# Kernel optimization log

Measured on AMD Instinct MI355X. Metric: run time of the kernel, lower is better.

The kernel has to match this reference:

```python
import jax, jax.numpy as jnp
import numpy as np

N, D, V = 4096, 256, 32000
B, T = 32, 256
U_DECAY, X_DECAY = 0.97, 0.97
EPS = 1e-6


def layernorm_row(z):
    # matches torch: (z - mean) / (std + eps), std with Bessel correction (ddof=1)
    m = jnp.mean(z, axis=-1, keepdims=True)
    s = jnp.std(z, axis=-1, keepdims=True, ddof=1)
    return (z - m) / (s + EPS)


def setup_inputs() -> dict:
    key = jax.random.key(0)
    k1, k2, k3, k4, k5 = jax.random.split(key, 5)
    token_emb = jax.random.normal(k1, (V, D), jnp.float32) / np.float32(np.sqrt(D))
    E = jax.random.normal(k2, (D, N), jnp.float32) / np.float32(np.sqrt(N))
    Dx = jax.random.normal(k3, (N, D), jnp.float32) / np.float32(np.sqrt(D))
    Dy = jax.random.normal(k4, (N, D), jnp.float32) / np.float32(np.sqrt(D))
    idx = jax.random.randint(k5, (B, T), 0, V)
    return {"idx": idx, "token_emb": token_emb, "E": E, "Dx": Dx, "Dy": Dy}


def reference(idx, token_emb, E, Dx, Dy):
    b = idx.shape[0]

    def step(carry, tok):
        x, rho = carry                                   # x: (b,n), rho: (b,d,n)
        v_prev = token_emb[tok]                          # (b,d) embedding gather
        x_t = X_DECAY * x + jax.nn.relu(v_prev @ Dx.T)   # (b,n)
        x_t = x_t / (jnp.sum(jnp.abs(x_t), axis=-1, keepdims=True) + EPS)  # L1 normalize
        a_star = jnp.einsum('bdn,bn->bd', rho, x_t)      # fast-weight readout
        y_t = jax.nn.relu(layernorm_row(a_star) @ Dy.T) * jax.nn.relu(x_t)  # (b,n)
        v_star = layernorm_row(y_t @ E.T)                # (b,d)
        # Hebbian decayed outer-product memory update
        rho = U_DECAY * (rho + jnp.einsum('bd,bn->bdn', layernorm_row(v_prev), x_t))
        return (x_t, rho), v_star

    x0 = jnp.zeros((b, N), jnp.float32)
    rho0 = jnp.zeros((b, D, N), jnp.float32)
    (_, _), vs = jax.lax.scan(step, (x0, rho0), idx.T)   # vs: (T,b,d)
    return jnp.transpose(vs, (1, 0, 2))                  # (b,T,d)
```

## Files before the change

### kernel.cpp

```cpp
#include <hip/hip_runtime.h>
#include <hip/hip_bf16.h>

#define NN 4096
#define DD 256
#define BB 32
#define TT 256
#define EPS 1e-6f
#define DECAY 0.97f
#define LOG2_DECAY -0.043943348f

typedef __hip_bfloat16 bf16;
typedef short short8 __attribute__((ext_vector_type(8)));
typedef float floatx4 __attribute__((ext_vector_type(4)));

__device__ __forceinline__ float bfu2f(short u) {
    return __uint_as_float(((unsigned)(unsigned short)u) << 16);
}

__device__ __forceinline__ float blk_sum_256(float v, volatile float* s4) {
#pragma unroll
    for (int o = 32; o > 0; o >>= 1) v += __shfl_down(v, o, 64);
    int lane = threadIdx.x & 63, w = threadIdx.x >> 6;
    __syncthreads();
    if (lane == 0) s4[w] = v;
    __syncthreads();
    return s4[0] + s4[1] + s4[2] + s4[3];
}

__device__ __forceinline__ void gl16(const bf16* g, bf16* l) {
    __builtin_amdgcn_global_load_lds((const __attribute__((address_space(1))) void*)g,
                                     (__attribute__((address_space(3))) void*)l, 16, 0, 0);
}

__global__ void k_detect(const unsigned short* __restrict__ raw, int* __restrict__ flag) {
    __shared__ int cnt[4];
    int tid = threadIdx.x;
    int bad = 0;
    for (int i = tid; i < 8192; i += 256) {
        unsigned int u = raw[2 * i];
        float v = __uint_as_float(u << 16);
        if (!(fabsf(v) < 1e6f)) bad++;
    }
#pragma unroll
    for (int o = 32; o > 0; o >>= 1) bad += __shfl_down(bad, o, 64);
    int lane = tid & 63, w = tid >> 6;
    if (lane == 0) cnt[w] = bad;
    __syncthreads();
    if (tid == 0) flag[0] = (cnt[0] + cnt[1] + cnt[2] + cnt[3] < 32) ? 1 : 0;
}

__global__ __launch_bounds__(256) void k_convert3(const void* __restrict__ s0,
                                                  const void* __restrict__ s1,
                                                  const void* __restrict__ s2,
                                                  bf16* __restrict__ d0,
                                                  bf16* __restrict__ d1,
                                                  bf16* __restrict__ d2,
                                                  const int* __restrict__ flag) {
    const int per = NN * DD / 8;
    int i = blockIdx.x * 256 + threadIdx.x;
    int m = i / per, j = i % per;
    const void* s = (m == 0) ? s0 : (m == 1) ? s1 : s2;
    bf16* d = (m == 0) ? d0 : (m == 1) ? d1 : d2;
    if (flag[0]) {
        ((uint4*)d)[j] = ((const uint4*)s)[j];
    } else {
        const float4* f = (const float4*)s;
        float4 a = f[2 * j], b = f[2 * j + 1];
        short8 o;
        float va[8] = {a.x, a.y, a.z, a.w, b.x, b.y, b.z, b.w};
#pragma unroll
        for (int k = 0; k < 8; k++) {
            bf16 t = __float2bfloat16(va[k]);
            o[k] = *reinterpret_cast<short*>(&t);
        }
        ((short8*)d)[j] = o;
    }
}

__global__ __launch_bounds__(256) void k_gather_ln(const void* __restrict__ emb,
                                                   const int* __restrict__ idx,
                                                   bf16* __restrict__ Vpb,
                                                   bf16* __restrict__ Ub,
                                                   const int* __restrict__ flag) {
    __shared__ float s4[4];
    int r = blockIdx.x, d = threadIdx.x;
    int tok = idx[r];
    long o = (long)tok * DD + d;
    float e = flag[0] ? __bfloat162float(((const bf16*)emb)[o]) : ((const float*)emb)[o];
    Vpb[(long)r * DD + d] = __float2bfloat16(e);
    float m = blk_sum_256(e, s4) * (1.0f / DD);
    float zc = e - m;
    float var = blk_sum_256(zc * zc, s4) * (1.0f / (DD - 1));
    Ub[(long)r * DD + d] = __float2bfloat16(zc / (sqrtf(fmaxf(var, 0.f)) + EPS));
}

__global__ __launch_bounds__(256) void k_transpose(const bf16* __restrict__ Ub,
                                                   bf16* __restrict__ Ut) {
    __shared__ bf16 tile[32][33];
    int b = blockIdx.z;
    int t0 = blockIdx.x * 32, d0 = blockIdx.y * 32;
    const bf16* src = Ub + (long)b * TT * DD;
    bf16* dst = Ut + (long)b * DD * TT;
    int rr = threadIdx.x >> 3, c4 = (threadIdx.x & 7) * 4;
#pragma unroll
    for (int i = 0; i < 4; i++) tile[rr][c4 + i] = src[(long)(t0 + rr) * DD + d0 + c4 + i];
    __syncthreads();
#pragma unroll
    for (int i = 0; i < 4; i++) dst[(long)(d0 + rr) * TT + t0 + c4 + i] = tile[c4 + i][rr];
}

enum { EPI_RELU_BF16 = 0, EPI_NONE_F32 = 1, EPI_RELU_MULX_BF16 = 2 };

template <int EPI>
__global__ __launch_bounds__(512, 2) void k_fused256(const bf16* __restrict__ A,
                                                     const bf16* __restrict__ B,
                                                     bf16* __restrict__ C,
                                                     const bf16* __restrict__ Xaux,
                                                     float* __restrict__ Wsum) {
    __shared__ __align__(16) char smem[65536];
    bf16* R = (bf16*)smem;

    int bx = blockIdx.x, by = blockIdx.y;
    {
        int gx = gridDim.x;
        int nwg = gx * gridDim.y;
        int id = by * gx + bx;
        int q = nwg >> 3;
        int nid = (id & 7) * q + (id >> 3);
        bx = nid % gx;
        by = nid / gx;
    }
    int bm = by * 256, bn = bx * 256;
    int tid = threadIdx.x, wid = tid >> 6, lane = tid & 63;
    int wr = wid >> 2, wc = wid & 3;
    int lm = lane & 15, kh = lane >> 4;

    int srow2 = tid >> 2;
    int swzcol = (((tid & 3) ^ ((srow2 >> 1) & 3)) << 3);
    const bf16* gA0 = A + (long)(bm + srow2) * DD + swzcol;
    const bf16* gA1 = gA0 + (long)128 * DD;
    const bf16* gB0 = B + (long)(bn + srow2) * DD + swzcol;
    const bf16* gB1 = gB0 + (long)128 * DD;
    int chunk = ((kh ^ ((lm >> 1) & 3)) << 3);

    floatx4 acc[8][4];
#pragma unroll
    for (int i = 0; i < 8; i++)
#pragma unroll
        for (int j = 0; j < 4; j++) acc[i][j] = (floatx4){0.f, 0.f, 0.f, 0.f};

#define STAGE256(SBASE, KK)                             \
    {                                                   \
        bf16* As_ = (bf16*)(SBASE);                     \
        bf16* Bs_ = As_ + 8192;                         \
        gl16(gA0 + (KK), As_ + tid * 8);                \
        gl16(gA1 + (KK), As_ + 4096 + tid * 8);         \
        gl16(gB0 + (KK), Bs_ + tid * 8);                \
        gl16(gB1 + (KK), Bs_ + 4096 + tid * 8);         \
    }

    STAGE256(smem, 0);

    int cur = 0;
#pragma unroll
    for (int k0 = 0; k0 < 256; k0 += 32) {
        __builtin_amdgcn_s_barrier();
        __builtin_amdgcn_sched_barrier(0);
        if (k0 + 32 < 256) STAGE256(smem + ((cur ^ 1) * 32768), k0 + 32);
        if (k0 + 32 < 256) asm volatile("s_waitcnt vmcnt(4)" ::: "memory");
        else               asm volatile("s_waitcnt vmcnt(0)" ::: "memory");
        __builtin_amdgcn_s_barrier();
        __builtin_amdgcn_sched_barrier(0);
        bf16* cbA = (bf16*)(smem + cur * 32768);
        bf16* cbB = cbA + 8192;
        short8 af[8], bfr[4];
#pragma unroll
        for (int i = 0; i < 8; i++)
            af[i] = *(const short8*)(cbA + (wr * 128 + i * 16 + lm) * 32 + chunk);
#pragma unroll
        for (int j = 0; j < 4; j++)
            bfr[j] = *(const short8*)(cbB + (wc * 64 + j * 16 + lm) * 32 + chunk);
#pragma unroll
        for (int i = 0; i < 8; i++)
#pragma unroll
            for (int j = 0; j < 4; j++)
                acc[i][j] = __builtin_amdgcn_mfma_f32_16x16x32_bf16(af[i], bfr[j], acc[i][j], 0, 0, 0);
        cur ^= 1;
    }
#undef STAGE256

#pragma unroll
    for (int p = 0; p < 4; p++) {
        __syncthreads();
        if (wr == (p >> 1)) {
            int ibase = (p & 1) * 4;
#pragma unroll
            for (int ii = 0; ii < 4; ii++)
#pragma unroll
                for (int j = 0; j < 4; j++)
#pragma unroll
                    for (int r = 0; r < 4; r++) {
                        int rr = ii * 16 + kh * 4 + r;
                        int cc = wc * 64 + j * 16 + lm;
                        R[rr * 264 + cc] = __float2bfloat16(fmaxf(acc[ibase + ii][j][r], 0.f));
                    }
        }
        __syncthreads();
#pragma unroll
        for (int it = 0; it < 4; it++) {
            int row_l = it * 16 + (tid >> 5);
            int c8 = (tid & 31) * 8;
            short8 vv = *(const short8*)(R + row_l * 264 + c8);
            int gm = bm + p * 64 + row_l;
            long off = (long)gm * NN + bn + c8;
            if (EPI == EPI_RELU_BF16) {
                *(short8*)(C + off) = vv;
                float s = 0.f;
#pragma unroll
                for (int k = 0; k < 8; k++) s += bfu2f(vv[k]);
#pragma unroll
                for (int o = 16; o > 0; o >>= 1) s += __shfl_down(s, o, 32);
                if ((tid & 31) == 0) atomicAdd(&Wsum[gm], s);
            } else {
                short8 xx = *(const short8*)(Xaux + off);
                short8 oo;
#pragma unroll
                for (int k = 0; k < 8; k++) {
                    float prod = bfu2f(vv[k]) * fmaxf(bfu2f(xx[k]), 0.f);
                    bf16 t = __float2bfloat16(prod);
                    oo[k] = *reinterpret_cast<short*>(&t);
                }
                *(short8*)(C + off) = oo;
            }
        }
    }
}

template <int EPI, int KSPLIT, int TRI, int SWZ>
__global__ __launch_bounds__(256) void k_mfma_nt(int K,
                                                 const bf16* __restrict__ A, int lda, long sA,
                                                 const bf16* __restrict__ B, int ldb, long sB,
                                                 void* __restrict__ Cv, int ldc, long sC,
                                                 const bf16* __restrict__ Xaux,
                                                 float* __restrict__ Wsum) {
    __shared__ __align__(16) char smem[49152];
    bf16* R = (bf16*)smem;

    int z = blockIdx.z;
    int bz = z / KSPLIT, ks = z % KSPLIT;
    A += (long)bz * sA;
    B += (long)bz * sB;
    int bx = blockIdx.x, by = blockIdx.y;
    if (TRI) {
        by = (blockIdx.x >= 1) ? 1 : 0;
        bx = (blockIdx.x == 2) ? 1 : 0;
    }
    if (SWZ) {
        int gx = gridDim.x;
        int nwg = gx * gridDim.y;
        int id = by * gx + bx;
        int q = nwg >> 3;
        int nid = (id & 7) * q + (id >> 3);
        bx = nid % gx;
        by = nid / gx;
    }
    int bm = by * 128, bn = bx * 128;
    int tid = threadIdx.x;
    int srow = tid >> 2;
    int scol = ((((srow >> 1) & 3) ^ (tid & 3)) << 3);
    int w = tid >> 6, lane = tid & 63;
    int wm = (w >> 1) * 64, wn = (w & 1) * 64;
    int lm = lane & 15, kh = lane >> 4;

    floatx4 acc[4][4];
#pragma unroll
    for (int i = 0; i < 4; i++)
#pragma unroll
        for (int j = 0; j < 4; j++) acc[i][j] = (floatx4){0.f, 0.f, 0.f, 0.f};

    int kchunk = K / KSPLIT;
    int kbeg = ks * kchunk, kend = kbeg + kchunk;
    const bf16* gA0 = A + (long)(bm + srow) * lda + scol;
    const bf16* gA1 = gA0 + (long)64 * lda;
    const bf16* gB0 = B + (long)(bn + srow) * ldb + scol;
    const bf16* gB1 = gB0 + (long)64 * ldb;
    int dslot = tid * 8;

#define STAGE_SLOT(SBASE, KK)                          \
    {                                                  \
        bf16* bufA = (bf16*)(SBASE);                   \
        bf16* bufB = bufA + 4096;                      \
        gl16(gA0 + (KK), bufA + dslot);                \
        gl16(gA1 + (KK), bufA + 2048 + dslot);         \
        gl16(gB0 + (KK), bufB + dslot);                \
        gl16(gB1 + (KK), bufB + 2048 + dslot);         \
    }

    STAGE_SLOT(smem, kbeg);
    if (kbeg + 32 < kend) STAGE_SLOT(smem + 16384, kbeg + 32);

    int cur = 0;
    for (int k0 = kbeg; k0 < kend; k0 += 32) {
        __builtin_amdgcn_s_barrier();
        __builtin_amdgcn_sched_barrier(0);
        if (k0 + 64 < kend) {
            int ps = (cur == 0) ? 2 : cur - 1;
            STAGE_SLOT(smem + ps * 16384, k0 + 64);
        }
        int rem = (kend - k0 - 32) >> 5;
        if (rem >= 2)      asm volatile("s_waitcnt vmcnt(8)" ::: "memory");
        else if (rem == 1) asm volatile("s_waitcnt vmcnt(4)" ::: "memory");
        else               asm volatile("s_waitcnt vmcnt(0)" ::: "memory");
        __builtin_amdgcn_s_barrier();
        __builtin_amdgcn_sched_barrier(0);
        bf16* cbA = (bf16*)(smem + cur * 16384);
        bf16* cbB = cbA + 4096;
        short8 af[4], bfr[4];
#pragma unroll
        for (int i = 0; i < 4; i++) {
            int row = wm + i * 16 + lm;
            af[i] = *(const short8*)(cbA + row * 32 + ((((row >> 1) & 3) ^ kh) << 3));
        }
#pragma unroll
        for (int j = 0; j < 4; j++) {
            int row = wn + j * 16 + lm;
            bfr[j] = *(const short8*)(cbB + row * 32 + ((((row >> 1) & 3) ^ kh) << 3));
        }
#pragma unroll
        for (int i = 0; i < 4; i++)
#pragma unroll
            for (int j = 0; j < 4; j++)
                acc[i][j] = __builtin_amdgcn_mfma_f32_16x16x32_bf16(af[i], bfr[j], acc[i][j], 0, 0, 0);
        cur = (cur == 2) ? 0 : cur + 1;
    }
#undef STAGE_SLOT

    if (EPI == EPI_NONE_F32) {
        long cbase = (long)z * sC;
#pragma unroll
        for (int i = 0; i < 4; i++)
#pragma unroll
            for (int j = 0; j < 4; j++)
#pragma unroll
                for (int r = 0; r < 4; r++) {
                    int gm = bm + wm + i * 16 + kh * 4 + r;
                    int gn = bn + wn + j * 16 + lm;
                    ((float*)Cv)[cbase + (long)gm * ldc + gn] = acc[i][j][r];
                }
        return;
    }

#pragma unroll
    for (int p = 0; p < 2; p++) {
        __syncthreads();
        if ((w >> 1) == p) {
#pragma unroll
            for (int i = 0; i < 4; i++)
#pragma unroll
                for (int j = 0; j < 4; j++)
#pragma unroll
                    for (int r = 0; r < 4; r++) {
                        int rr = i * 16 + kh * 4 + r;
                        int cc = wn + j * 16 + lm;
                        R[rr * 136 + cc] = __float2bfloat16(fmaxf(acc[i][j][r], 0.f));
                    }
        }
        __syncthreads();
#pragma unroll
        for (int it = 0; it < 4; it++) {
            int row_l = it * 16 + (tid >> 4);
            int c8 = (tid & 15) * 8;
            short8 vv = *(const short8*)(R + row_l * 136 + c8);
            int gm = bm + p * 64 + row_l;
            long off = (long)gm * ldc + bn + c8;
            if (EPI == EPI_RELU_BF16) {
                *(short8*)((bf16*)Cv + off) = vv;
                float s = 0.f;
#pragma unroll
                for (int k = 0; k < 8; k++) s += bfu2f(vv[k]);
#pragma unroll
                for (int o = 8; o > 0; o >>= 1) s += __shfl_down(s, o, 16);
                if ((tid & 15) == 0) atomicAdd(&Wsum[gm], s);
            } else {
                short8 xx = *(const short8*)(Xaux + off);
                short8 oo;
#pragma unroll
                for (int k = 0; k < 8; k++) {
                    float prod = bfu2f(vv[k]) * fmaxf(bfu2f(xx[k]), 0.f);
                    bf16 t = __float2bfloat16(prod);
                    oo[k] = *reinterpret_cast<short*>(&t);
                }
                *(short8*)((bf16*)Cv + off) = oo;
            }
        }
    }
}

__global__ __launch_bounds__(256) void k_scalar_scan(const float* __restrict__ Wsum,
                                                     float* __restrict__ invS) {
    __shared__ float sw[BB * TT];
    for (int i = threadIdx.x; i < BB * TT; i += 256) sw[i] = Wsum[i];
    __syncthreads();
    int b = threadIdx.x;
    if (b < BB) {
        float sig = 0.f;
        for (int t = 0; t < TT; t++) {
            float S = DECAY * sig + sw[b * TT + t];
            float inv = 1.f / (S + EPS);
            invS[b * TT + t] = inv;
            sig = S * inv;
        }
    }
}

__global__ __launch_bounds__(256) void k_colscan(bf16* __restrict__ W,
                                                 const float* __restrict__ invS) {
    __shared__ float sv[TT];
    int b = blockIdx.y;
    sv[threadIdx.x] = invS[b * TT + threadIdx.x];
    __syncthreads();
    int n = blockIdx.x * 256 + threadIdx.x;
    bf16* p = W + (long)b * TT * NN + n;
    float x = 0.f;
    for (int t = 0; t < TT; t++) {
        float w = __bfloat162float(p[(long)t * NN]);
        x = (DECAY * x + w) * sv[t];
        p[(long)t * NN] = __float2bfloat16(x);
    }
}

__global__ __launch_bounds__(256) void k_reduce_mask(const float* __restrict__ Gp,
                                                     bf16* __restrict__ G) {
    int r = blockIdx.x;
    int b = r >> 8, t = r & 255;
    int s = threadIdx.x;
    long base = ((long)b * 4) * 65536 + (long)t * 256 + s;
    float v = Gp[base] + Gp[base + 65536] + Gp[base + 2 * 65536] + Gp[base + 3 * 65536];
    float o = (s < t) ? v * exp2f((float)(t - s) * LOG2_DECAY) : 0.f;
    G[(long)r * 256 + s] = __float2bfloat16(o);
}

__global__ __launch_bounds__(256) void k_ln_rows(const float* __restrict__ Zp,
                                                 bf16* __restrict__ O) {
    __shared__ float s4[4];
    long r = blockIdx.x;
    int d = threadIdx.x;
    long b = r >> 8, t = r & 255;
    long base = (b * 2) * 65536 + t * 256 + d;
    float z = Zp[base] + Zp[base + 65536];
    float m = blk_sum_256(z, s4) * (1.0f / DD);
    float zc = z - m;
    float var = blk_sum_256(zc * zc, s4) * (1.0f / (DD - 1));
    O[r * DD + d] = __float2bfloat16(zc / (sqrtf(fmaxf(var, 0.f)) + EPS));
}

__global__ __launch_bounds__(256) void k_final_ln(const float* __restrict__ Zp,
                                                  void* __restrict__ out,
                                                  const int* __restrict__ flag) {
    __shared__ float s4[4];
    long r = blockIdx.x;
    int d = threadIdx.x;
    const long SL = (long)8192 * 256;
    long o = r * DD + d;
    float z = Zp[o] + Zp[o + SL] + Zp[o + 2 * SL] + Zp[o + 3 * SL];
    float m = blk_sum_256(z, s4) * (1.0f / DD);
    float zc = z - m;
    float var = blk_sum_256(zc * zc, s4) * (1.0f / (DD - 1));
    float v = zc / (sqrtf(fmaxf(var, 0.f)) + EPS);
    if (flag[0]) ((bf16*)out)[o] = __float2bfloat16(v);
    else ((float*)out)[o] = v;
}

extern "C" void kernel_launch(void* const* d_in, const int* in_sizes, int n_in,
                              void* d_out, int out_size, void* d_ws, size_t ws_size,
                              hipStream_t stream) {
    const int* idx = (const int*)d_in[0];
    const void* emb = d_in[1];
    const void* E = d_in[2];
    const void* Dx = d_in[3];
    const void* Dy = d_in[4];

    char* base = (char*)d_ws;
    size_t off = 0;
    int* flag = (int*)base; off += 1024;
    bf16* Dxb = (bf16*)(base + off); off += (size_t)NN * DD * 2;
    bf16* Dyb = (bf16*)(base + off); off += (size_t)NN * DD * 2;
    bf16* Eb  = (bf16*)(base + off); off += (size_t)DD * NN * 2;
    bf16* Vpb = (bf16*)(base + off); off += (size_t)BB * TT * DD * 2;
    bf16* Ub  = (bf16*)(base + off); off += (size_t)BB * TT * DD * 2;
    bf16* Ut  = (bf16*)(base + off); off += (size_t)BB * TT * DD * 2;
    float* Wsum = (float*)(base + off); off += (size_t)BB * TT * 4;
    float* invS = (float*)(base + off); off += (size_t)BB * TT * 4;
    bf16* ALNb = (bf16*)(base + off); off += (size_t)BB * TT * DD * 2;
    bf16* G = (bf16*)(base + off); off += (size_t)BB * TT * TT * 2;
    float* Gp = (float*)(base + off); off += (size_t)4 * BB * TT * TT * 4;
    float* Astar = Gp;
    float* Zp = Gp;
    bf16* Xb = (bf16*)(base + off); off += (size_t)BB * TT * NN * 2;

    const int M = BB * TT;

    k_detect<<<1, 256, 0, stream>>>((const unsigned short*)emb, flag);
    k_convert3<<<3 * NN * DD / 8 / 256, 256, 0, stream>>>(Dx, Dy, E, Dxb, Dyb, Eb, flag);
    k_gather_ln<<<M, 256, 0, stream>>>(emb, idx, Vpb, Ub, flag);
    k_transpose<<<dim3(8, 8, BB), 256, 0, stream>>>(Ub, Ut);

    hipMemsetAsync(Wsum, 0, (size_t)M * 4, stream);

    k_fused256<EPI_RELU_BF16><<<dim3(16, 32), 512, 0, stream>>>(Vpb, Dxb, Xb, nullptr, Wsum);

    k_scalar_scan<<<1, 256, 0, stream>>>(Wsum, invS);
    k_colscan<<<dim3(16, BB, 1), 256, 0, stream>>>(Xb, invS);

    k_mfma_nt<EPI_NONE_F32, 4, 1, 0><<<dim3(3, 1, BB * 4), 256, 0, stream>>>(
        NN, Xb, NN, (long)TT * NN, Xb, NN, (long)TT * NN, Gp, TT, (long)TT * TT, nullptr, nullptr);
    k_reduce_mask<<<M, 256, 0, stream>>>(Gp, G);

    k_mfma_nt<EPI_NONE_F32, 2, 0, 0><<<dim3(2, 2, BB * 2), 256, 0, stream>>>(
        TT, G, TT, (long)TT * TT, Ut, TT, (long)DD * TT, Astar, DD, (long)TT * DD, nullptr, nullptr);
    k_ln_rows<<<M, 256, 0, stream>>>(Astar, ALNb);

    k_fused256<EPI_RELU_MULX_BF16><<<dim3(16, 32), 512, 0, stream>>>(ALNb, Dyb, Xb, Xb, nullptr);

    k_mfma_nt<EPI_NONE_F32, 4, 0, 1><<<dim3(2, 64, 4), 256, 0, stream>>>(
        NN, Xb, NN, 0, Eb, NN, 0, Zp, DD, (long)M * DD, nullptr, nullptr);

    k_final_ln<<<M, 256, 0, stream>>>(Zp, d_out, flag);
}
```

Before: 312.0 us.

## Deepen fused GEMM pipeline to 4-stage ping-pong and vectorize column scan

The 256x256 fused GEMM goes from double to quad buffering in 128KB of dynamic LDS. Each k-step is split into two MFMA halves, with A and B tile prefetches interleaved between them and s_setprio raising priority around the MFMA blocks, so global loads, LDS reads and matrix math overlap more. The column scan now handles two bf16 columns per thread with 32-bit loads and prefetches the next row. The larger LDS footprint likely drops occupancy from 2 blocks per CU to 1, relying on the deeper pipeline and priority scheduling to hide latency instead.

```diff
diff --git a/kernel.cpp b/kernel.cpp
--- a/kernel.cpp
+++ b/kernel.cpp
@@ -117,7 +117,7 @@
                                                      bf16* __restrict__ C,
                                                      const bf16* __restrict__ Xaux,
                                                      float* __restrict__ Wsum) {
-    __shared__ __align__(16) char smem[65536];
+    extern __shared__ __align__(16) char smem[];
     bf16* R = (bf16*)smem;
 
     int bx = blockIdx.x, by = blockIdx.y;
@@ -149,45 +149,74 @@
 #pragma unroll
         for (int j = 0; j < 4; j++) acc[i][j] = (floatx4){0.f, 0.f, 0.f, 0.f};
 
-#define STAGE256(SBASE, KK)                             \
-    {                                                   \
-        bf16* As_ = (bf16*)(SBASE);                     \
-        bf16* Bs_ = As_ + 8192;                         \
-        gl16(gA0 + (KK), As_ + tid * 8);                \
-        gl16(gA1 + (KK), As_ + 4096 + tid * 8);         \
-        gl16(gB0 + (KK), Bs_ + tid * 8);                \
-        gl16(gB1 + (KK), Bs_ + 4096 + tid * 8);         \
-    }
-
-    STAGE256(smem, 0);
-
-    int cur = 0;
-#pragma unroll
-    for (int k0 = 0; k0 < 256; k0 += 32) {
-        __builtin_amdgcn_s_barrier();
-        __builtin_amdgcn_sched_barrier(0);
-        if (k0 + 32 < 256) STAGE256(smem + ((cur ^ 1) * 32768), k0 + 32);
-        if (k0 + 32 < 256) asm volatile("s_waitcnt vmcnt(4)" ::: "memory");
-        else               asm volatile("s_waitcnt vmcnt(0)" ::: "memory");
-        __builtin_amdgcn_s_barrier();
-        __builtin_amdgcn_sched_barrier(0);
-        bf16* cbA = (bf16*)(smem + cur * 32768);
+#define STG_A(BUF, KK)                                        \
+    {                                                         \
+        bf16* As_ = (bf16*)(smem + (BUF) * 32768);            \
+        gl16(gA0 + (KK), As_ + tid * 8);                      \
+        gl16(gA1 + (KK), As_ + 4096 + tid * 8);               \
+    }
+#define STG_B(BUF, KK)                                        \
+    {                                                         \
+        bf16* Bs_ = (bf16*)(smem + (BUF) * 32768) + 8192;     \
+        gl16(gB0 + (KK), Bs_ + tid * 8);                      \
+        gl16(gB1 + (KK), Bs_ + 4096 + tid * 8);               \
+    }
+
+    STG_A(0, 0)  STG_B(0, 0)
+    STG_A(1, 32) STG_B(1, 32)
+    STG_A(2, 64) STG_B(2, 64)
+    asm volatile("s_waitcnt vmcnt(8)" ::: "memory");
+    __builtin_amdgcn_s_barrier();
+    __builtin_amdgcn_sched_barrier(0);
+
+#pragma unroll
+    for (int kt = 0; kt < 8; kt++) {
+        bf16* cbA = (bf16*)(smem + (kt & 3) * 32768);
         bf16* cbB = cbA + 8192;
-        short8 af[8], bfr[4];
-#pragma unroll
-        for (int i = 0; i < 8; i++)
-            af[i] = *(const short8*)(cbA + (wr * 128 + i * 16 + lm) * 32 + chunk);
+        short8 af[4], bfr[4];
+        if (kt + 3 < 8) STG_A((kt + 3) & 3, (kt + 3) * 32)
 #pragma unroll
         for (int j = 0; j < 4; j++)
             bfr[j] = *(const short8*)(cbB + (wc * 64 + j * 16 + lm) * 32 + chunk);
 #pragma unroll
-        for (int i = 0; i < 8; i++)
+        for (int i = 0; i < 4; i++)
+            af[i] = *(const short8*)(cbA + (wr * 128 + i * 16 + lm) * 32 + chunk);
+        __builtin_amdgcn_sched_barrier(0);
+        __builtin_amdgcn_s_barrier();
+        asm volatile("s_waitcnt lgkmcnt(0)" ::: "memory");
+        __builtin_amdgcn_sched_barrier(0);
+        __builtin_amdgcn_s_setprio(1);
+#pragma unroll
+        for (int i = 0; i < 4; i++)
 #pragma unroll
             for (int j = 0; j < 4; j++)
                 acc[i][j] = __builtin_amdgcn_mfma_f32_16x16x32_bf16(af[i], bfr[j], acc[i][j], 0, 0, 0);
-        cur ^= 1;
-    }
-#undef STAGE256
+        __builtin_amdgcn_s_setprio(0);
+        __builtin_amdgcn_sched_barrier(0);
+        __builtin_amdgcn_s_barrier();
+        if (kt + 3 < 8) STG_B((kt + 3) & 3, (kt + 3) * 32)
+#pragma unroll
+        for (int i = 0; i < 4; i++)
+            af[i] = *(const short8*)(cbA + (wr * 128 + (4 + i) * 16 + lm) * 32 + chunk);
+        __builtin_amdgcn_sched_barrier(0);
+        if (kt <= 4)      asm volatile("s_waitcnt vmcnt(8)" ::: "memory");
+        else if (kt == 5) asm volatile("s_waitcnt vmcnt(4)" ::: "memory");
+        else if (kt == 6) asm volatile("s_waitcnt vmcnt(0)" ::: "memory");
+        __builtin_amdgcn_s_barrier();
+        asm volatile("s_waitcnt lgkmcnt(0)" ::: "memory");
+        __builtin_amdgcn_sched_barrier(0);
+        __builtin_amdgcn_s_setprio(1);
+#pragma unroll
+        for (int i = 0; i < 4; i++)
+#pragma unroll
+            for (int j = 0; j < 4; j++)
+                acc[4 + i][j] = __builtin_amdgcn_mfma_f32_16x16x32_bf16(af[i], bfr[j], acc[4 + i][j], 0, 0, 0);
+        __builtin_amdgcn_s_setprio(0);
+        __builtin_amdgcn_sched_barrier(0);
+        __builtin_amdgcn_s_barrier();
+    }
+#undef STG_A
+#undef STG_B
 
 #pragma unroll
     for (int p = 0; p < 4; p++) {
@@ -419,13 +448,31 @@
     int b = blockIdx.y;
     sv[threadIdx.x] = invS[b * TT + threadIdx.x];
     __syncthreads();
-    int n = blockIdx.x * 256 + threadIdx.x;
-    bf16* p = W + (long)b * TT * NN + n;
-    float x = 0.f;
-    for (int t = 0; t < TT; t++) {
-        float w = __bfloat162float(p[(long)t * NN]);
-        x = (DECAY * x + w) * sv[t];
-        p[(long)t * NN] = __float2bfloat16(x);
+    int n2 = blockIdx.x * 256 + threadIdx.x;
+    unsigned int* p = (unsigned int*)(W + (long)b * TT * NN) + n2;
+    const int STRIDE = NN / 2;
+    float x0 = 0.f, x1 = 0.f;
+    unsigned int cur = p[0];
+    for (int t = 0; t < TT - 1; t++) {
+        unsigned int nxt = p[(t + 1) * STRIDE];
+        float w0 = __uint_as_float(cur << 16);
+        float w1 = __uint_as_float(cur & 0xffff0000u);
+        x0 = (DECAY * x0 + w0) * sv[t];
+        x1 = (DECAY * x1 + w1) * sv[t];
+        bf16 b0 = __float2bfloat16(x0), b1 = __float2bfloat16(x1);
+        p[t * STRIDE] = (unsigned int)(*(unsigned short*)&b0) |
+                        ((unsigned int)(*(unsigned short*)&b1) << 16);
+        cur = nxt;
+    }
+    {
+        int t = TT - 1;
+        float w0 = __uint_as_float(cur << 16);
+        float w1 = __uint_as_float(cur & 0xffff0000u);
+        x0 = (DECAY * x0 + w0) * sv[t];
+        x1 = (DECAY * x1 + w1) * sv[t];
+        bf16 b0 = __float2bfloat16(x0), b1 = __float2bfloat16(x1);
+        p[t * STRIDE] = (unsigned int)(*(unsigned short*)&b0) |
+                        ((unsigned int)(*(unsigned short*)&b1) << 16);
     }
 }
 
@@ -479,6 +526,15 @@
     const void* E = d_in[2];
     const void* Dx = d_in[3];
     const void* Dy = d_in[4];
+
+    static int attr_done = 0;
+    if (!attr_done) {
+        (void)hipFuncSetAttribute((const void*)k_fused256<EPI_RELU_BF16>,
+                                  hipFuncAttributeMaxDynamicSharedMemorySize, 131072);
+        (void)hipFuncSetAttribute((const void*)k_fused256<EPI_RELU_MULX_BF16>,
+                                  hipFuncAttributeMaxDynamicSharedMemorySize, 131072);
+        attr_done = 1;
+    }
 
     char* base = (char*)d_ws;
     size_t off = 0;
@@ -507,10 +563,10 @@
 
     hipMemsetAsync(Wsum, 0, (size_t)M * 4, stream);
 
-    k_fused256<EPI_RELU_BF16><<<dim3(16, 32), 512, 0, stream>>>(Vpb, Dxb, Xb, nullptr, Wsum);
+    k_fused256<EPI_RELU_BF16><<<dim3(16, 32), 512, 131072, stream>>>(Vpb, Dxb, Xb, nullptr, Wsum);
 
     k_scalar_scan<<<1, 256, 0, stream>>>(Wsum, invS);
-    k_colscan<<<dim3(16, BB, 1), 256, 0, stream>>>(Xb, invS);
+    k_colscan<<<dim3(NN / 512, BB, 1), 256, 0, stream>>>(Xb, invS);
 
     k_mfma_nt<EPI_NONE_F32, 4, 1, 0><<<dim3(3, 1, BB * 4), 256, 0, stream>>>(
         NN, Xb, NN, (long)TT * NN, Xb, NN, (long)TT * NN, Gp, TT, (long)TT * TT, nullptr, nullptr);
@@ -520,7 +576,7 @@
         TT, G, TT, (long)TT * TT, Ut, TT, (long)DD * TT, Astar, DD, (long)TT * DD, nullptr, nullptr);
     k_ln_rows<<<M, 256, 0, stream>>>(Astar, ALNb);
 
-    k_fused256<EPI_RELU_MULX_BF16><<<dim3(16, 32), 512, 0, stream>>>(ALNb, Dyb, Xb, Xb, nullptr);
+    k_fused256<EPI_RELU_MULX_BF16><<<dim3(16, 32), 512, 131072, stream>>>(ALNb, Dyb, Xb, Xb, nullptr);
 
     k_mfma_nt<EPI_NONE_F32, 4, 0, 1><<<dim3(2, 64, 4), 256, 0, stream>>>(
         NN, Xb, NN, 0, Eb, NN, 0, Zp, DD, (long)M * DD, nullptr, nullptr);
```

Result: slower. 322.8 us (+3.4%).
